# Kernel optimization log

Measured on AMD Instinct MI355X. Metric: run time of the kernel, lower is better.

The kernel has to match this reference:

```python
import jax, jax.numpy as jnp
import numpy as np

EPS = 1e-5

def _ln(x, g, b):
    mu = x.mean(-1, keepdims=True)
    v = x.var(-1, keepdims=True)
    return g * (x - mu) / jnp.sqrt(v + EPS) + b

def _mlp(x, W0, b0, g0, be0, W1, b1, g1, be1, W2, b2, nm):
    # Linear -> LN -> GELU, Linear -> LN -> GELU, Linear -> split into complex
    h = jax.nn.gelu(_ln(x @ W0 + b0, g0, be0), approximate=False)
    h = jax.nn.gelu(_ln(h @ W1 + b1, g1, be1), approximate=False)
    o = h @ W2 + b2
    return jax.lax.complex(o[..., :nm], o[..., nm:])

def _forward(x, w_W0, w_b0, w_g0, w_be0, w_W1, w_b1, w_g1, w_be1, w_W2, w_b2,
             h_W0, h_b0, h_g0, h_be0, h_W1, h_b1, h_g1, h_be1, h_W2, h_b2,
             freq_r, freq_i, mixer_w, mixer_b, norm_g, norm_b, sc_w, sc_b):
    B, C, H, W = x.shape
    m1, m2 = freq_r.shape[2], freq_r.shape[3]
    wc = jnp.linspace(0.0, 1.0, W, dtype=x.dtype)
    hc = jnp.linspace(0.0, 1.0, H, dtype=x.dtype)
    # W-basis conditioned on values and normalized w-coordinate
    x_nhwc = x.transpose(0, 2, 3, 1)                                   # (B,H,W,C)
    w_in = jnp.concatenate([x_nhwc, jnp.broadcast_to(wc[None, None, :, None], (B, H, W, 1))], -1)
    wb = _mlp(w_in, w_W0, w_b0, w_g0, w_be0, w_W1, w_b1, w_g1, w_be1, w_W2, w_b2, m2)  # (B,H,W,m2) c64
    xc = x.astype(jnp.complex64)
    t = jnp.einsum('bchw,bhwm->bchm', xc, wb)                          # (B,C,H,m2)
    # H-basis conditioned on real part of W-transformed signal
    h_in = jnp.concatenate([t.real.transpose(0, 3, 2, 1),
                            jnp.broadcast_to(hc[None, None, :, None], (B, m2, H, 1))], -1)
    hb = _mlp(h_in, h_W0, h_b0, h_g0, h_be0, h_W1, h_b1, h_g1, h_be1, h_W2, h_b2, m1)  # (B,m2,H,m1)
    t2 = jnp.einsum('bchm,bmhn->bcnm', t, hb)                          # (B,C,m1,m2)
    Wf = jax.lax.complex(freq_r, freq_i)                               # (C,O,m1,m2)
    proc = jnp.einsum('bixy,oixy->boxy', t2, Wf)                       # (B,O,m1,m2)
    # Inverse transforms via conjugate-transposed bases
    rec_h = jnp.einsum('bonm,bmhn->bohm', proc, jnp.conj(hb))          # (B,O,H,m2)
    rec = jnp.einsum('bohm,bhwm->bohw', rec_h, jnp.conj(wb))           # (B,O,H,W)
    y = rec.real / (H * W)
    y = jnp.einsum('bchw,oc->bohw', y, mixer_w) + mixer_b[None, :, None, None]
    mu = y.mean(1, keepdims=True)
    v = y.var(1, keepdims=True)
    y = norm_g[None, :, None, None] * (y - mu) / jnp.sqrt(v + EPS) + norm_b[None, :, None, None]
    y = jax.nn.gelu(y, approximate=False)
    sc = jnp.einsum('bchw,oc->bohw', x, sc_w) + sc_b[None, :, None, None]
    return jax.nn.gelu(y + sc, approximate=False)

def setup_inputs() -> dict:
    key = jax.random.key(0)
    B, C, O, H, W, M1, M2, HD = 8, 64, 64, 192, 192, 48, 48, 64
    ks = jax.random.split(key, 12)
    r = lambda k, sh, s=0.05: jax.random.normal(k, sh, jnp.float32) * s
    d = dict(x=jax.random.normal(ks[0], (B, C, H, W), jnp.float32))
    d.update(w_W0=r(ks[1], (C + 1, HD)), w_b0=jnp.zeros(HD), w_g0=jnp.ones(HD), w_be0=jnp.zeros(HD),
             w_W1=r(ks[2], (HD, HD)), w_b1=jnp.zeros(HD), w_g1=jnp.ones(HD), w_be1=jnp.zeros(HD),
             w_W2=r(ks[3], (HD, 2 * M2)), w_b2=jnp.zeros(2 * M2))
    d.update(h_W0=r(ks[4], (C + 1, HD)), h_b0=jnp.zeros(HD), h_g0=jnp.ones(HD), h_be0=jnp.zeros(HD),
             h_W1=r(ks[5], (HD, HD)), h_b1=jnp.zeros(HD), h_g1=jnp.ones(HD), h_be1=jnp.zeros(HD),
             h_W2=r(ks[6], (HD, 2 * M1)), h_b2=jnp.zeros(2 * M1))
    d.update(freq_r=r(ks[7], (C, O, M1, M2), 0.1), freq_i=r(ks[8], (C, O, M1, M2), 0.1),
             mixer_w=r(ks[9], (O, O)), mixer_b=jnp.zeros(O),
             norm_g=jnp.ones(O), norm_b=jnp.zeros(O),
             sc_w=r(ks[10], (O, C)), sc_b=jnp.zeros(O))
    return d

def reference(x, w_W0, w_b0, w_g0, w_be0, w_W1, w_b1, w_g1, w_be1, w_W2, w_b2,
              h_W0, h_b0, h_g0, h_be0, h_W1, h_b1, h_g1, h_be1, h_W2, h_b2,
              freq_r, freq_i, mixer_w, mixer_b, norm_g, norm_b, sc_w, sc_b):
    return _forward(x, w_W0, w_b0, w_g0, w_be0, w_W1, w_b1, w_g1, w_be1, w_W2, w_b2,
                    h_W0, h_b0, h_g0, h_be0, h_W1, h_b1, h_g1, h_be1, h_W2, h_b2,
                    freq_r, freq_i, mixer_w, mixer_b, norm_g, norm_b, sc_w, sc_b)
```

## Files before the change

kernel.cpp:

```cpp
#include <hip/hip_runtime.h>
#include <math.h>

#define LN_EPS 1e-5f

typedef short bf16x8 __attribute__((ext_vector_type(8)));
typedef float f32x4  __attribute__((ext_vector_type(4)));

__device__ __forceinline__ float gelu_f(float v) {
    return 0.5f * v * (1.0f + erff(v * 0.70710678118654752f));
}
__device__ __forceinline__ unsigned short f2bf(float f) {
    unsigned u = __float_as_uint(f);
    return (unsigned short)((u + 0x7fffu + ((u >> 16) & 1u)) >> 16);
}
__device__ __forceinline__ float bf2f(unsigned short h) {
    return __uint_as_float(((unsigned)h) << 16);
}

__global__ __launch_bounds__(256) void k0_swizzle(
    const float* __restrict__ wW0, const float* __restrict__ wW1, const float* __restrict__ wW2,
    const float* __restrict__ hW0, const float* __restrict__ hW1, const float* __restrict__ hW2,
    uint4* __restrict__ dst)
{
    int mat = blockIdx.x;
    const float* W; int N, ntiles, base;
    switch (mat) {
      case 0: W=wW0; N=64; ntiles=8;  base=0;    break;
      case 1: W=wW1; N=64; ntiles=8;  base=1024; break;
      case 2: W=wW2; N=96; ntiles=12; base=2048; break;
      case 3: W=hW0; N=64; ntiles=8;  base=3584; break;
      case 4: W=hW1; N=64; ntiles=8;  base=4608; break;
      default:W=hW2; N=96; ntiles=12; base=5632; break;
    }
    int lane = threadIdx.x & 63;
    for (int t = threadIdx.x >> 6; t < ntiles; t += 4) {
        int nt = t >> 1, ks = t & 1;
        int n  = nt*16 + (lane & 15);
        int k0 = ks*32 + (lane >> 4)*8;
        unsigned hi[8], lo[8];
        #pragma unroll
        for (int j = 0; j < 8; ++j) {
            float v = W[(k0 + j)*N + n];
            unsigned short h = f2bf(v);
            hi[j] = h;
            lo[j] = f2bf(v - bf2f(h));
        }
        uint4 ph, pl;
        ph.x = hi[0] | (hi[1]<<16); ph.y = hi[2] | (hi[3]<<16);
        ph.z = hi[4] | (hi[5]<<16); ph.w = hi[6] | (hi[7]<<16);
        pl.x = lo[0] | (lo[1]<<16); pl.y = lo[2] | (lo[3]<<16);
        pl.z = lo[4] | (lo[5]<<16); pl.w = lo[6] | (lo[7]<<16);
        dst[base + t*128 + lane]      = ph;
        dst[base + t*128 + 64 + lane] = pl;
    }
}

__global__ __launch_bounds__(256) void k0b_swizzle(
    const float* __restrict__ mw, const float* __restrict__ sw,
    uint4* __restrict__ dst)
{
    int mat = blockIdx.x;
    const float* W = mat ? sw : mw;
    int base = mat ? 1024 : 0;
    int lane = threadIdx.x & 63;
    for (int t = threadIdx.x >> 6; t < 8; t += 4) {
        int nt = t >> 1, ks = t & 1;
        int n  = nt*16 + (lane & 15);
        int k0 = ks*32 + (lane >> 4)*8;
        unsigned hi[8], lo[8];
        #pragma unroll
        for (int j = 0; j < 8; ++j) {
            float v = W[n*64 + (k0 + j)];
            unsigned short h = f2bf(v);
            hi[j] = h;
            lo[j] = f2bf(v - bf2f(h));
        }
        uint4 ph, pl;
        ph.x = hi[0] | (hi[1]<<16); ph.y = hi[2] | (hi[3]<<16);
        ph.z = hi[4] | (hi[5]<<16); ph.w = hi[6] | (hi[7]<<16);
        pl.x = lo[0] | (lo[1]<<16); pl.y = lo[2] | (lo[3]<<16);
        pl.z = lo[4] | (lo[5]<<16); pl.w = lo[6] | (lo[7]<<16);
        dst[base + t*128 + lane]      = ph;
        dst[base + t*128 + 64 + lane] = pl;
    }
}

template<int NT, int STRIDE>
__device__ __forceinline__ void gemm64s(
    const unsigned short* aHi, const unsigned short* aLo,
    const uint4* __restrict__ wsw, int tbase, int row, int quad, int lane,
    f32x4* acc)
{
    union U { uint4 u; bf16x8 b; };
    bf16x8 aH[2], aL[2];
    #pragma unroll
    for (int ks = 0; ks < 2; ++ks) {
        aH[ks] = *(const bf16x8*)&aHi[row*STRIDE + ks*32 + quad*8];
        aL[ks] = *(const bf16x8*)&aLo[row*STRIDE + ks*32 + quad*8];
    }
    #pragma unroll
    for (int nt = 0; nt < NT; ++nt) {
        f32x4 a = {0.f, 0.f, 0.f, 0.f};
        #pragma unroll
        for (int ks = 0; ks < 2; ++ks) {
            int t = tbase + nt*2 + ks;
            U bh, bl;
            bh.u = wsw[t*128 + lane];
            bl.u = wsw[t*128 + 64 + lane];
            a = __builtin_amdgcn_mfma_f32_16x16x32_bf16(aH[ks], bh.b, a, 0, 0, 0);
            a = __builtin_amdgcn_mfma_f32_16x16x32_bf16(aH[ks], bl.b, a, 0, 0, 0);
            a = __builtin_amdgcn_mfma_f32_16x16x32_bf16(aL[ks], bh.b, a, 0, 0, 0);
        }
        acc[nt] = a;
    }
}

template<int NT>
__device__ __forceinline__ void gemm64(
    const unsigned short* aHi, const unsigned short* aLo,
    const uint4* __restrict__ wsw, int tbase, int row, int quad, int lane,
    f32x4* acc)
{
    gemm64s<NT, 72>(aHi, aLo, wsw, tbase, row, quad, lane, acc);
}

__device__ __forceinline__ void ln_gelu_pass(
    f32x4* acc, const float* __restrict__ bias, const float* __restrict__ wrow,
    float coordBase, float coordScale,
    const float* __restrict__ gg, const float* __restrict__ bb,
    unsigned short* aHi, unsigned short* aLo, int rbase, int quad, int li)
{
    float vals[4][4];
    float s1[4] = {0,0,0,0}, s2[4] = {0,0,0,0};
    #pragma unroll
    for (int nt = 0; nt < 4; ++nt) {
        int col = nt*16 + li;
        float bv = bias[col];
        float br = wrow[col];
        #pragma unroll
        for (int rg = 0; rg < 4; ++rg) {
            float coord = (coordBase + (float)(rbase + quad*4 + rg)) * coordScale;
            float v = acc[nt][rg] + fmaf(coord, br, bv);
            vals[nt][rg] = v;
            s1[rg] += v;
            s2[rg] = fmaf(v, v, s2[rg]);
        }
    }
    #pragma unroll
    for (int d = 1; d < 16; d <<= 1) {
        #pragma unroll
        for (int rg = 0; rg < 4; ++rg) {
            s1[rg] += __shfl_xor(s1[rg], d, 64);
            s2[rg] += __shfl_xor(s2[rg], d, 64);
        }
    }
    #pragma unroll
    for (int nt = 0; nt < 4; ++nt) {
        int col = nt*16 + li;
        float gv = gg[col], bev = bb[col];
        #pragma unroll
        for (int rg = 0; rg < 4; ++rg) {
            float mu   = s1[rg] * 0.015625f;
            float rstd = rsqrtf(s2[rg]*0.015625f - mu*mu + LN_EPS);
            float v = gelu_f(fmaf((vals[nt][rg] - mu)*rstd, gv, bev));
            int r = rbase + quad*4 + rg;
            unsigned short hv = f2bf(v);
            aHi[r*72 + col] = hv;
            aLo[r*72 + col] = f2bf(v - bf2f(hv));
        }
    }
}

__device__ __forceinline__ void mlp_body(
    unsigned short* aHi, unsigned short* aLo,
    const uint4* __restrict__ wsw,
    const float* __restrict__ w0row,
    const float* __restrict__ b0, const float* __restrict__ g0, const float* __restrict__ be0,
    const float* __restrict__ b1, const float* __restrict__ g1, const float* __restrict__ be1,
    const float* __restrict__ b2,
    float coordBase,
    float* __restrict__ outR, float* __restrict__ outI, int pixBase)
{
    int tid = threadIdx.x;
    int wv = __builtin_amdgcn_readfirstlane(tid >> 6);
    int lane = tid & 63, li = lane & 15, quad = lane >> 4;
    int rbase = wv*16;
    int row = rbase + li;
    f32x4 acc[6];

    gemm64<4>(aHi, aLo, wsw, 0, row, quad, lane, acc);
    ln_gelu_pass(acc, b0, w0row, coordBase, 1.0f/191.0f, g0, be0, aHi, aLo, rbase, quad, li);
    gemm64<4>(aHi, aLo, wsw, 8, row, quad, lane, acc);
    ln_gelu_pass(acc, b1, b1, 0.f, 0.f, g1, be1, aHi, aLo, rbase, quad, li);
    gemm64<6>(aHi, aLo, wsw, 16, row, quad, lane, acc);
    #pragma unroll
    for (int nt = 0; nt < 6; ++nt) {
        int j = nt*16 + li;
        float bv = b2[j];
        #pragma unroll
        for (int rg = 0; rg < 4; ++rg) {
            float v = acc[nt][rg] + bv;
            int pix = pixBase + rbase + quad*4 + rg;
            if (nt < 3) outR[pix*48 + j]        = v;
            else        outI[pix*48 + (j - 48)] = v;
        }
    }
}

__global__ __launch_bounds__(256) void k1_mlp_w(
    const float* __restrict__ x, const float* __restrict__ W0full,
    const float* __restrict__ b0, const float* __restrict__ g0, const float* __restrict__ be0,
    const float* __restrict__ b1, const float* __restrict__ g1, const float* __restrict__ be1,
    const float* __restrict__ b2,
    const uint4* __restrict__ wsw,
    float* __restrict__ wb_r, float* __restrict__ wb_i)
{
    __shared__ unsigned short aHi[64*72];
    __shared__ unsigned short aLo[64*72];
    int tid = threadIdx.x;
    int wv = __builtin_amdgcn_readfirstlane(tid >> 6);
    int lane = tid & 63, li = lane & 15, quad = lane >> 4;
    int wq = blockIdx.x % 3;
    int bh = blockIdx.x / 3;
    int b = bh / 192, h = bh % 192;
    int w0 = wq * 64;
    int r = wv*16 + li;
    #pragma unroll
    for (int cc = 0; cc < 16; ++cc) {
        int c = cc*4 + quad;
        float v = x[((b*64 + c)*192 + h)*192 + (w0 + r)];
        unsigned short hv = f2bf(v);
        aHi[r*72 + c] = hv;
        aLo[r*72 + c] = f2bf(v - bf2f(hv));
    }
    mlp_body(aHi, aLo, wsw, W0full + 64*64, b0, g0, be0, b1, g1, be1, b2,
             (float)w0, wb_r, wb_i, bh*192 + w0);
}

__global__ __launch_bounds__(256) void k3_mlp_h(
    const float* __restrict__ t_r, const float* __restrict__ W0full,
    const float* __restrict__ b0, const float* __restrict__ g0, const float* __restrict__ be0,
    const float* __restrict__ b1, const float* __restrict__ g1, const float* __restrict__ be1,
    const float* __restrict__ b2,
    const uint4* __restrict__ wsw,
    float* __restrict__ hb_r, float* __restrict__ hb_i)
{
    __shared__ unsigned short aHi[64*72];
    __shared__ unsigned short aLo[64*72];
    int tid = threadIdx.x;
    int wv = __builtin_amdgcn_readfirstlane(tid >> 6);
    int lane = tid & 63, li = lane & 15, quad = lane >> 4;
    int hq = blockIdx.x % 3;
    int bm = blockIdx.x / 3;
    int b = bm / 48, m = bm % 48;
    int h0 = hq * 64;
    int r = wv*16 + li;
    #pragma unroll
    for (int cc = 0; cc < 16; ++cc) {
        int c = cc*4 + quad;
        float v = t_r[((b*192 + h0 + r)*64 + c)*48 + m];
        unsigned short hv = f2bf(v);
        aHi[r*72 + c] = hv;
        aLo[r*72 + c] = f2bf(v - bf2f(hv));
    }
    mlp_body(aHi, aLo, wsw, W0full + 64*64, b0, g0, be0, b1, g1, be1, b2,
             (float)h0, hb_r, hb_i, bm*192 + h0);
}

__global__ __launch_bounds__(256) void k2_t(
    const float* __restrict__ x,
    const float* __restrict__ wb_r, const float* __restrict__ wb_i,
    float* __restrict__ t_r, float* __restrict__ t_i)
{
    __shared__ unsigned short aHi[64*72];
    __shared__ unsigned short aLo[64*72];
    __shared__ uint4 bfrag[1536];
    int bh = blockIdx.x;
    int b = bh / 192, h = bh % 192;
    int tid = threadIdx.x;
    int wv = __builtin_amdgcn_readfirstlane(tid >> 6);
    int lane = tid & 63, li = lane & 15, quad = lane >> 4;
    int rbase = wv*16;
    int row = rbase + li;

    f32x4 acc[6];
    {
        f32x4 z = {0.f, 0.f, 0.f, 0.f};
        #pragma unroll
        for (int nt = 0; nt < 6; ++nt) acc[nt] = z;
    }
    union U { uint4 u; bf16x8 b8; };

    for (int w0 = 0; w0 < 192; w0 += 64) {
        if (w0) __syncthreads();
        {
            const float4* srow = (const float4*)(x + ((b*64 + row)*192 + h)*192 + w0) + quad*4;
            #pragma unroll
            for (int q = 0; q < 4; ++q) {
                float4 v4 = srow[q];
                float vv[4] = {v4.x, v4.y, v4.z, v4.w};
                int k0 = quad*16 + q*4;
                #pragma unroll
                for (int e = 0; e < 4; ++e) {
                    unsigned short hv = f2bf(vv[e]);
                    aHi[row*72 + k0 + e] = hv;
                    aLo[row*72 + k0 + e] = f2bf(vv[e] - bf2f(hv));
                }
            }
        }
        for (int t = tid >> 6; t < 12; t += 4) {
            int nt = t >> 1, ks = t & 1;
            const float* src = (nt < 3) ? wb_r : wb_i;
            int col = (nt < 3 ? nt : nt - 3)*16 + li;
            const float* sp = src + (bh*192 + w0 + ks*32 + quad*8)*48 + col;
            unsigned hi8[8], lo8[8];
            #pragma unroll
            for (int j = 0; j < 8; ++j) {
                float v = sp[j*48];
                unsigned short hv = f2bf(v);
                hi8[j] = hv;
                lo8[j] = f2bf(v - bf2f(hv));
            }
            uint4 ph, pl;
            ph.x = hi8[0] | (hi8[1]<<16); ph.y = hi8[2] | (hi8[3]<<16);
            ph.z = hi8[4] | (hi8[5]<<16); ph.w = hi8[6] | (hi8[7]<<16);
            pl.x = lo8[0] | (lo8[1]<<16); pl.y = lo8[2] | (lo8[3]<<16);
            pl.z = lo8[4] | (lo8[5]<<16); pl.w = lo8[6] | (lo8[7]<<16);
            bfrag[t*64 + lane]       = ph;
            bfrag[768 + t*64 + lane] = pl;
        }
        __syncthreads();
        bf16x8 aH[2], aL[2];
        #pragma unroll
        for (int ks = 0; ks < 2; ++ks) {
            aH[ks] = *(const bf16x8*)&aHi[row*72 + ks*32 + quad*8];
            aL[ks] = *(const bf16x8*)&aLo[row*72 + ks*32 + quad*8];
        }
        #pragma unroll
        for (int nt = 0; nt < 6; ++nt) {
            f32x4 a = acc[nt];
            #pragma unroll
            for (int ks = 0; ks < 2; ++ks) {
                int t = nt*2 + ks;
                U bh_, bl_;
                bh_.u = bfrag[t*64 + lane];
                bl_.u = bfrag[768 + t*64 + lane];
                a = __builtin_amdgcn_mfma_f32_16x16x32_bf16(aH[ks], bh_.b8, a, 0, 0, 0);
                a = __builtin_amdgcn_mfma_f32_16x16x32_bf16(aH[ks], bl_.b8, a, 0, 0, 0);
                a = __builtin_amdgcn_mfma_f32_16x16x32_bf16(aL[ks], bh_.b8, a, 0, 0, 0);
            }
            acc[nt] = a;
        }
    }
    #pragma unroll
    for (int nt = 0; nt < 6; ++nt) {
        #pragma unroll
        for (int rg = 0; rg < 4; ++rg) {
            int c = rbase + quad*4 + rg;
            float v = acc[nt][rg];
            if (nt < 3) t_r[(bh*64 + c)*48 + nt*16 + li]       = v;
            else        t_i[(bh*64 + c)*48 + (nt - 3)*16 + li] = v;
        }
    }
}

__global__ __launch_bounds__(256) void k4_t2(
    const float* __restrict__ t_r, const float* __restrict__ t_i,
    const float* __restrict__ hb_r, const float* __restrict__ hb_i,
    float* __restrict__ t2_r, float* __restrict__ t2_i)
{
    __shared__ unsigned short aHi[64*72];
    __shared__ unsigned short aLo[64*72];
    __shared__ uint4 bfrag[1536];
    int bm = blockIdx.x;
    int b = bm / 48, m = bm % 48;
    int tid = threadIdx.x;
    int wv = __builtin_amdgcn_readfirstlane(tid >> 6);
    int lane = tid & 63, li = lane & 15, quad = lane >> 4;
    int rbase = wv*16;
    int row = rbase + li;

    f32x4 acc[6];
    {
        f32x4 z = {0.f, 0.f, 0.f, 0.f};
        #pragma unroll
        for (int nt = 0; nt < 6; ++nt) acc[nt] = z;
    }
    union U { uint4 u; bf16x8 b8; };

    for (int p = 0; p < 6; ++p) {
        bool realp = (p < 3);
        int h0 = (p % 3) * 64;
        if (p) __syncthreads();
        {
            const float* tsrc = (realp ? t_r : t_i)
                              + ((b*192 + h0)*64 + row)*48 + m;
            #pragma unroll
            for (int q = 0; q < 16; ++q) {
                int k = quad*16 + q;
                float v = tsrc[k*3072];
                unsigned short hv = f2bf(v);
                aHi[row*72 + k] = hv;
                aLo[row*72 + k] = f2bf(v - bf2f(hv));
            }
        }
        for (int t = tid >> 6; t < 12; t += 4) {
            int nt = t >> 1, ks = t & 1;
            const float* src;
            int col;
            float sgn = 1.f;
            if (realp) {
                if (nt < 3) { src = hb_r; col = nt*16 + li; }
                else        { src = hb_i; col = (nt - 3)*16 + li; }
            } else {
                if (nt < 3) { src = hb_i; col = nt*16 + li; sgn = -1.f; }
                else        { src = hb_r; col = (nt - 3)*16 + li; }
            }
            const float* sp = src + (bm*192 + h0 + ks*32 + quad*8)*48 + col;
            unsigned hi8[8], lo8[8];
            #pragma unroll
            for (int j = 0; j < 8; ++j) {
                float v = sgn * sp[j*48];
                unsigned short hv = f2bf(v);
                hi8[j] = hv;
                lo8[j] = f2bf(v - bf2f(hv));
            }
            uint4 ph, pl;
            ph.x = hi8[0] | (hi8[1]<<16); ph.y = hi8[2] | (hi8[3]<<16);
            ph.z = hi8[4] | (hi8[5]<<16); ph.w = hi8[6] | (hi8[7]<<16);
            pl.x = lo8[0] | (lo8[1]<<16); pl.y = lo8[2] | (lo8[3]<<16);
            pl.z = lo8[4] | (lo8[5]<<16); pl.w = lo8[6] | (lo8[7]<<16);
            bfrag[t*64 + lane]       = ph;
            bfrag[768 + t*64 + lane] = pl;
        }
        __syncthreads();
        bf16x8 aH[2], aL[2];
        #pragma unroll
        for (int ks = 0; ks < 2; ++ks) {
            aH[ks] = *(const bf16x8*)&aHi[row*72 + ks*32 + quad*8];
            aL[ks] = *(const bf16x8*)&aLo[row*72 + ks*32 + quad*8];
        }
        #pragma unroll
        for (int nt = 0; nt < 6; ++nt) {
            f32x4 a = acc[nt];
            #pragma unroll
            for (int ks = 0; ks < 2; ++ks) {
                int t = nt*2 + ks;
                U bh_, bl_;
                bh_.u = bfrag[t*64 + lane];
                bl_.u = bfrag[768 + t*64 + lane];
                a = __builtin_amdgcn_mfma_f32_16x16x32_bf16(aH[ks], bh_.b8, a, 0, 0, 0);
                a = __builtin_amdgcn_mfma_f32_16x16x32_bf16(aH[ks], bl_.b8, a, 0, 0, 0);
                a = __builtin_amdgcn_mfma_f32_16x16x32_bf16(aL[ks], bh_.b8, a, 0, 0, 0);
            }
            acc[nt] = a;
        }
    }
    #pragma unroll
    for (int nt = 0; nt < 6; ++nt) {
        #pragma unroll
        for (int rg = 0; rg < 4; ++rg) {
            int c = rbase + quad*4 + rg;
            float v = acc[nt][rg];
            if (nt < 3) t2_r[((b*64 + c)*48 + nt*16 + li)*48 + m]       = v;
            else        t2_i[((b*64 + c)*48 + (nt - 3)*16 + li)*48 + m] = v;
        }
    }
}

__global__ __launch_bounds__(256) void k5_proc(
    const float* __restrict__ t2_r, const float* __restrict__ t2_i,
    const float* __restrict__ fr, const float* __restrict__ fi,
    float* __restrict__ proc_r, float* __restrict__ proc_i)
{
    int og = blockIdx.x & 31;
    int ch = blockIdx.x >> 5;
    int nm = ch*256 + threadIdx.x;
    int o0 = og*2;
    float p0r[8], p0i[8], p1r[8], p1i[8];
    #pragma unroll
    for (int bb = 0; bb < 8; ++bb) { p0r[bb]=0.f; p0i[bb]=0.f; p1r[bb]=0.f; p1i[bb]=0.f; }
    for (int i = 0; i < 64; ++i) {
        float w0r = fr[(o0*64 + i)*2304 + nm];
        float w0i = fi[(o0*64 + i)*2304 + nm];
        float w1r = fr[((o0+1)*64 + i)*2304 + nm];
        float w1i = fi[((o0+1)*64 + i)*2304 + nm];
        #pragma unroll
        for (int bb = 0; bb < 8; ++bb) {
            float tr = t2_r[(bb*64 + i)*2304 + nm];
            float ti = t2_i[(bb*64 + i)*2304 + nm];
            p0r[bb] = fmaf(tr, w0r, fmaf(-ti, w0i, p0r[bb]));
            p0i[bb] = fmaf(tr, w0i, fmaf( ti, w0r, p0i[bb]));
            p1r[bb] = fmaf(tr, w1r, fmaf(-ti, w1i, p1r[bb]));
            p1i[bb] = fmaf(tr, w1i, fmaf( ti, w1r, p1i[bb]));
        }
    }
    #pragma unroll
    for (int bb = 0; bb < 8; ++bb) {
        proc_r[(bb*64 + o0)*2304 + nm]     = p0r[bb];
        proc_i[(bb*64 + o0)*2304 + nm]     = p0i[bb];
        proc_r[(bb*64 + o0 + 1)*2304 + nm] = p1r[bb];
        proc_i[(bb*64 + o0 + 1)*2304 + nm] = p1i[bb];
    }
}

__global__ __launch_bounds__(256) void k6_rech(
    const float* __restrict__ proc_r, const float* __restrict__ proc_i,
    const float* __restrict__ hb_r, const float* __restrict__ hb_i,
    float* __restrict__ rh_r, float* __restrict__ rh_i)
{
    __shared__ unsigned short aHi[64*104];
    __shared__ unsigned short aLo[64*104];
    __shared__ uint4 bfrag[1536];
    int hq = blockIdx.x % 3;
    int bm = blockIdx.x / 3;
    int b = bm / 48, m = bm % 48;
    int h0 = hq * 64;
    int tid = threadIdx.x;
    int wv = __builtin_amdgcn_readfirstlane(tid >> 6);
    int lane = tid & 63, li = lane & 15, quad = lane >> 4;
    int rbase = wv*16;
    int row = rbase + li;

    {
        int hr = bm*192 + h0 + row;
        const float4* pr = (const float4*)(hb_r + hr*48) + quad*3;
        const float4* pi = (const float4*)(hb_i + hr*48) + quad*3;
        #pragma unroll
        for (int q = 0; q < 3; ++q) {
            float4 vr = pr[q];
            float4 vi = pi[q];
            int k0 = quad*12 + q*4;
            float vs[8] = {vr.x, vr.y, vr.z, vr.w, vi.x, vi.y, vi.z, vi.w};
            #pragma unroll
            for (int e = 0; e < 4; ++e) {
                unsigned short h1 = f2bf(vs[e]);
                aHi[row*104 + k0 + e] = h1;
                aLo[row*104 + k0 + e] = f2bf(vs[e] - bf2f(h1));
                unsigned short h2 = f2bf(vs[4+e]);
                aHi[row*104 + 48 + k0 + e] = h2;
                aLo[row*104 + 48 + k0 + e] = f2bf(vs[4+e] - bf2f(h2));
            }
        }
    }
    union U { uint4 u; bf16x8 b8; };
    bf16x8 aH[3], aL[3];
    #pragma unroll
    for (int ks = 0; ks < 3; ++ks) {
        aH[ks] = *(const bf16x8*)&aHi[row*104 + ks*32 + quad*8];
        aL[ks] = *(const bf16x8*)&aLo[row*104 + ks*32 + quad*8];
    }

    f32x4 accR[4], accI[4];
    for (int pass = 0; pass < 2; ++pass) {
        if (pass) __syncthreads();
        for (int t = tid >> 6; t < 12; t += 4) {
            int ks = t % 3;
            int nt = t / 3;
            int o = nt*16 + li;
            const float* base_lo = pass ? proc_i : proc_r;
            const float* base_hi = pass ? proc_r : proc_i;
            float sgn_hi = pass ? -1.f : 1.f;
            unsigned hi8[8], lo8[8];
            #pragma unroll
            for (int j = 0; j < 8; ++j) {
                int kk = ks*32 + quad*8 + j;
                float v;
                if (kk < 48) v = base_lo[(b*64 + o)*2304 + kk*48 + m];
                else         v = sgn_hi * base_hi[(b*64 + o)*2304 + (kk - 48)*48 + m];
                unsigned short hv = f2bf(v);
                hi8[j] = hv;
                lo8[j] = f2bf(v - bf2f(hv));
            }
            uint4 ph, pl;
            ph.x = hi8[0] | (hi8[1]<<16); ph.y = hi8[2] | (hi8[3]<<16);
            ph.z = hi8[4] | (hi8[5]<<16); ph.w = hi8[6] | (hi8[7]<<16);
            pl.x = lo8[0] | (lo8[1]<<16); pl.y = lo8[2] | (lo8[3]<<16);
            pl.z = lo8[4] | (lo8[5]<<16); pl.w = lo8[6] | (lo8[7]<<16);
            bfrag[t*64 + lane]       = ph;
            bfrag[768 + t*64 + lane] = pl;
        }
        __syncthreads();
        f32x4* acc = pass ? accI : accR;
        #pragma unroll
        for (int nt = 0; nt < 4; ++nt) {
            f32x4 a = {0.f, 0.f, 0.f, 0.f};
            #pragma unroll
            for (int ks = 0; ks < 3; ++ks) {
                int t = nt*3 + ks;
                U bh_, bl_;
                bh_.u = bfrag[t*64 + lane];
                bl_.u = bfrag[768 + t*64 + lane];
                a = __builtin_amdgcn_mfma_f32_16x16x32_bf16(aH[ks], bh_.b8, a, 0, 0, 0);
                a = __builtin_amdgcn_mfma_f32_16x16x32_bf16(aH[ks], bl_.b8, a, 0, 0, 0);
                a = __builtin_amdgcn_mfma_f32_16x16x32_bf16(aL[ks], bh_.b8, a, 0, 0, 0);
            }
            acc[nt] = a;
        }
    }
    #pragma unroll
    for (int nt = 0; nt < 4; ++nt) {
        int o = nt*16 + li;
        #pragma unroll
        for (int rg = 0; rg < 4; ++rg) {
            int hrow = h0 + rbase + quad*4 + rg;
            int a = (bm*192 + hrow)*64 + o;
            rh_r[a] = accR[nt][rg];
            rh_i[a] = accI[nt][rg];
        }
    }
}

__global__ __launch_bounds__(256) void k7_rec(
    const float* __restrict__ rh_r, const float* __restrict__ rh_i,
    const float* __restrict__ wb_r, const float* __restrict__ wb_i,
    const float* __restrict__ x,
    const uint4* __restrict__ msw,
    const float* __restrict__ mb,
    const float* __restrict__ nrm_g, const float* __restrict__ nrm_b,
    const float* __restrict__ sb,
    float* __restrict__ out)
{
    __shared__ unsigned short aHi[64*104];
    __shared__ unsigned short aLo[64*104];
    __shared__ uint4 bfrag[1536];
    float* cbuf = (float*)bfrag;

    int wq = blockIdx.x % 3;
    int bh = blockIdx.x / 3;
    int b = bh / 192, h = bh % 192;
    int w0 = wq * 64;
    int tid = threadIdx.x;
    int wv = __builtin_amdgcn_readfirstlane(tid >> 6);
    int lane = tid & 63, li = lane & 15, quad = lane >> 4;
    int rbase = wv*16;
    int row = rbase + li;

    {
        int pix = bh*192 + w0 + row;
        const float4* pr = (const float4*)(wb_r + pix*48) + quad*3;
        const float4* pi = (const float4*)(wb_i + pix*48) + quad*3;
        #pragma unroll
        for (int q = 0; q < 3; ++q) {
            float4 vr = pr[q];
            float4 vi = pi[q];
            int k0 = quad*12 + q*4;
            float vs[8] = {vr.x, vr.y, vr.z, vr.w, vi.x, vi.y, vi.z, vi.w};
            #pragma unroll
            for (int e = 0; e < 4; ++e) {
                unsigned short h1 = f2bf(vs[e]);
                aHi[row*104 + k0 + e] = h1;
                aLo[row*104 + k0 + e] = f2bf(vs[e] - bf2f(h1));
                unsigned short h2 = f2bf(vs[4+e]);
                aHi[row*104 + 48 + k0 + e] = h2;
                aLo[row*104 + 48 + k0 + e] = f2bf(vs[4+e] - bf2f(h2));
            }
        }
    }
    for (int t = tid >> 6; t < 12; t += 4) {
        int ks = t % 3;
        int nt = t / 3;
        int o = nt*16 + li;
        unsigned hi8[8], lo8[8];
        #pragma unroll
        for (int j = 0; j < 8; ++j) {
            int kk = ks*32 + quad*8 + j;
            const float* src = (kk < 48) ? rh_r : rh_i;
            int m = (kk < 48) ? kk : kk - 48;
            float v = src[((b*48 + m)*192 + h)*64 + o];
            unsigned short hv = f2bf(v);
            hi8[j] = hv;
            lo8[j] = f2bf(v - bf2f(hv));
        }
        uint4 ph, pl;
        ph.x = hi8[0] | (hi8[1]<<16); ph.y = hi8[2] | (hi8[3]<<16);
        ph.z = hi8[4] | (hi8[5]<<16); ph.w = hi8[6] | (hi8[7]<<16);
        pl.x = lo8[0] | (lo8[1]<<16); pl.y = lo8[2] | (lo8[3]<<16);
        pl.z = lo8[4] | (lo8[5]<<16); pl.w = lo8[6] | (lo8[7]<<16);
        bfrag[t*64 + lane]       = ph;
        bfrag[768 + t*64 + lane] = pl;
    }
    __syncthreads();

    union U { uint4 u; bf16x8 b; };
    bf16x8 aH[3], aL[3];
    #pragma unroll
    for (int ks = 0; ks < 3; ++ks) {
        aH[ks] = *(const bf16x8*)&aHi[row*104 + ks*32 + quad*8];
        aL[ks] = *(const bf16x8*)&aLo[row*104 + ks*32 + quad*8];
    }
    f32x4 acc[4];
    #pragma unroll
    for (int nt = 0; nt < 4; ++nt) {
        f32x4 a = {0.f, 0.f, 0.f, 0.f};
        #pragma unroll
        for (int ks = 0; ks < 3; ++ks) {
            int t = nt*3 + ks;
            U bh_, bl_;
            bh_.u = bfrag[t*64 + lane];
            bl_.u = bfrag[768 + t*64 + lane];
            a = __builtin_amdgcn_mfma_f32_16x16x32_bf16(aH[ks], bh_.b, a, 0, 0, 0);
            a = __builtin_amdgcn_mfma_f32_16x16x32_bf16(aH[ks], bl_.b, a, 0, 0, 0);
            a = __builtin_amdgcn_mfma_f32_16x16x32_bf16(aL[ks], bh_.b, a, 0, 0, 0);
        }
        acc[nt] = a;
    }

    const float s = 1.0f / 36864.0f;
    #pragma unroll
    for (int nt = 0; nt < 4; ++nt) {
        int o = nt*16 + li;
        #pragma unroll
        for (int rg = 0; rg < 4; ++rg) {
            int prow = rbase + quad*4 + rg;
            float v = acc[nt][rg] * s;
            unsigned short hv = f2bf(v);
            aHi[prow*104 + o] = hv;
            aLo[prow*104 + o] = f2bf(v - bf2f(hv));
        }
    }
    f32x4 accy[4];
    gemm64s<4, 104>(aHi, aLo, msw, 0, row, quad, lane, accy);

    float vals[4][4];
    float s1[4] = {0,0,0,0}, s2[4] = {0,0,0,0};
    #pragma unroll
    for (int nt = 0; nt < 4; ++nt) {
        int o = nt*16 + li;
        float bv = mb[o];
        #pragma unroll
        for (int rg = 0; rg < 4; ++rg) {
            float v = accy[nt][rg] + bv;
            vals[nt][rg] = v;
            s1[rg] += v;
            s2[rg] = fmaf(v, v, s2[rg]);
        }
    }
    #pragma unroll
    for (int d = 1; d < 16; d <<= 1) {
        #pragma unroll
        for (int rg = 0; rg < 4; ++rg) {
            s1[rg] += __shfl_xor(s1[rg], d, 64);
            s2[rg] += __shfl_xor(s2[rg], d, 64);
        }
    }

    #pragma unroll
    for (int cc = 0; cc < 16; ++cc) {
        int c = cc*4 + quad;
        float v = x[((b*64 + c)*192 + h)*192 + w0 + row];
        unsigned short hv = f2bf(v);
        aHi[row*104 + c] = hv;
        aLo[row*104 + c] = f2bf(v - bf2f(hv));
    }
    gemm64s<4, 104>(aHi, aLo, msw, 8, row, quad, lane, acc);

    __syncthreads();
    #pragma unroll
    for (int nt = 0; nt < 4; ++nt) {
        int o = nt*16 + li;
        float gv = nrm_g[o], bev = nrm_b[o], sbv = sb[o];
        #pragma unroll
        for (int rg = 0; rg < 4; ++rg) {
            float mu   = s1[rg] * 0.015625f;
            float rstd = rsqrtf(s2[rg]*0.015625f - mu*mu + LN_EPS);
            float v  = gelu_f(fmaf((vals[nt][rg] - mu)*rstd, gv, bev));
            float sc = acc[nt][rg] + sbv;
            int prow = rbase + quad*4 + rg;
            cbuf[prow*67 + o] = gelu_f(v + sc);
        }
    }
    __syncthreads();
    #pragma unroll
    for (int it = 0; it < 16; ++it) {
        int o = it*4 + (tid >> 6);
        int pix = tid & 63;
        out[((b*64 + o)*192 + h)*192 + w0 + pix] = cbuf[pix*67 + o];
    }
}

extern "C" void kernel_launch(void* const* d_in, const int* in_sizes, int n_in,
                              void* d_out, int out_size, void* d_ws, size_t ws_size,
                              hipStream_t stream)
{
    (void)in_sizes; (void)n_in; (void)out_size; (void)ws_size;
    const float* x    = (const float*)d_in[0];
    const float* wW0  = (const float*)d_in[1];
    const float* wb0  = (const float*)d_in[2];
    const float* wg0  = (const float*)d_in[3];
    const float* wbe0 = (const float*)d_in[4];
    const float* wW1  = (const float*)d_in[5];
    const float* wb1  = (const float*)d_in[6];
    const float* wg1  = (const float*)d_in[7];
    const float* wbe1 = (const float*)d_in[8];
    const float* wW2  = (const float*)d_in[9];
    const float* wb2  = (const float*)d_in[10];
    const float* hW0  = (const float*)d_in[11];
    const float* hb0  = (const float*)d_in[12];
    const float* hg0  = (const float*)d_in[13];
    const float* hbe0 = (const float*)d_in[14];
    const float* hW1  = (const float*)d_in[15];
    const float* hb1  = (const float*)d_in[16];
    const float* hg1  = (const float*)d_in[17];
    const float* hbe1 = (const float*)d_in[18];
    const float* hW2  = (const float*)d_in[19];
    const float* hb2  = (const float*)d_in[20];
    const float* fr   = (const float*)d_in[21];
    const float* fi   = (const float*)d_in[22];
    const float* mw   = (const float*)d_in[23];
    const float* mb   = (const float*)d_in[24];
    const float* ngp  = (const float*)d_in[25];
    const float* nbp  = (const float*)d_in[26];
    const float* sw   = (const float*)d_in[27];
    const float* sb   = (const float*)d_in[28];
    float* out = (float*)d_out;

    float* ws   = (float*)d_ws;
    float* wbr  = ws;
    float* wbi  = ws + 14155776;
    float* t_r  = ws + 28311552;
    float* t_i  = ws + 33030144;
    float* hbr  = ws + 37748736;
    float* hbi  = ws + 41287680;
    float* t2r  = ws + 44826624;
    float* t2i  = ws + 46006272;
    float* prr  = ws + 47185920;
    float* pri  = ws + 48365568;
    float* rhr  = t_r;
    float* rhi  = t_i;
    float* wswb = ws + 49545216;
    uint4* wsw  = (uint4*)wswb;
    uint4* msw  = (uint4*)t2r;

    k0_swizzle<<<dim3(6), dim3(256), 0, stream>>>(wW0, wW1, wW2, hW0, hW1, hW2, wsw);
    k1_mlp_w<<<dim3(4608), dim3(256), 0, stream>>>(x, wW0, wb0, wg0, wbe0,
                                                   wb1, wg1, wbe1, wb2, wsw, wbr, wbi);
    k2_t<<<dim3(1536), dim3(256), 0, stream>>>(x, wbr, wbi, t_r, t_i);
    k3_mlp_h<<<dim3(1152), dim3(256), 0, stream>>>(t_r, hW0, hb0, hg0, hbe0,
                                                   hb1, hg1, hbe1, hb2, wsw + 3584, hbr, hbi);
    k4_t2<<<dim3(384), dim3(256), 0, stream>>>(t_r, t_i, hbr, hbi, t2r, t2i);
    k5_proc<<<dim3(288), dim3(256), 0, stream>>>(t2r, t2i, fr, fi, prr, pri);
    k0b_swizzle<<<dim3(2), dim3(256), 0, stream>>>(mw, sw, msw);
    k6_rech<<<dim3(1152), dim3(256), 0, stream>>>(prr, pri, hbr, hbi, rhr, rhi);
    k7_rec<<<dim3(4608), dim3(256), 0, stream>>>(rhr, rhi, wbr, wbi,
                                                 x, msw, mb, ngp, nbp, sb, out);
}
```

Measured before the change: 685.0 us.

## Transpose t and proc intermediate layouts for coalesced loads downstream

Changes the storage layout of the intermediate t (now b,m,h,c) and proc (now b,m,o,n) so that the consumers k3, k4 and k6 read contiguous data, using float4 loads in k3 and k6. k2 now stages its output through shared memory, reusing the bfrag buffer, so its writes into the new layout stay coalesced. k5 writes proc with a strided pattern in exchange. The aim is to remove the heavily strided gathers in the MLP-H, t2 and rec_h kernels, at the cost of extra barriers in k2 and less coalesced stores in k5.

New measurement: 567.8 us. 17.1% less time.

```diff
diff --git a/kernel.cpp b/kernel.cpp
--- a/kernel.cpp
+++ b/kernel.cpp
@@ -255,13 +255,20 @@
     int b = bm / 48, m = bm % 48;
     int h0 = hq * 64;
     int r = wv*16 + li;
-    #pragma unroll
-    for (int cc = 0; cc < 16; ++cc) {
-        int c = cc*4 + quad;
-        float v = t_r[((b*192 + h0 + r)*64 + c)*48 + m];
-        unsigned short hv = f2bf(v);
-        aHi[r*72 + c] = hv;
-        aLo[r*72 + c] = f2bf(v - bf2f(hv));
+    {
+        const float4* tb = (const float4*)(t_r + ((b*48 + m)*192 + h0 + r)*64);
+        #pragma unroll
+        for (int q = 0; q < 4; ++q) {
+            float4 v4 = tb[quad*4 + q];
+            float vv[4] = {v4.x, v4.y, v4.z, v4.w};
+            int k0 = quad*16 + q*4;
+            #pragma unroll
+            for (int e = 0; e < 4; ++e) {
+                unsigned short hv = f2bf(vv[e]);
+                aHi[r*72 + k0 + e] = hv;
+                aLo[r*72 + k0 + e] = f2bf(vv[e] - bf2f(hv));
+            }
+        }
     }
     mlp_body(aHi, aLo, wsw, W0full + 64*64, b0, g0, be0, b1, g1, be1, b2,
              (float)h0, hb_r, hb_i, bm*192 + h0);
@@ -275,6 +282,7 @@
     __shared__ unsigned short aHi[64*72];
     __shared__ unsigned short aLo[64*72];
     __shared__ uint4 bfrag[1536];
+    float* cbuf = (float*)bfrag;
     int bh = blockIdx.x;
     int b = bh / 192, h = bh % 192;
     int tid = threadIdx.x;
@@ -352,15 +360,35 @@
             acc[nt] = a;
         }
     }
-    #pragma unroll
-    for (int nt = 0; nt < 6; ++nt) {
+    __syncthreads();
+    #pragma unroll
+    for (int nt = 0; nt < 3; ++nt) {
+        int m = nt*16 + li;
         #pragma unroll
         for (int rg = 0; rg < 4; ++rg) {
             int c = rbase + quad*4 + rg;
-            float v = acc[nt][rg];
-            if (nt < 3) t_r[(bh*64 + c)*48 + nt*16 + li]       = v;
-            else        t_i[(bh*64 + c)*48 + (nt - 3)*16 + li] = v;
-        }
+            cbuf[m*67 + c] = acc[nt][rg];
+        }
+    }
+    __syncthreads();
+    for (int idx = tid; idx < 3072; idx += 256) {
+        int m = idx >> 6, c = idx & 63;
+        t_r[((b*48 + m)*192 + h)*64 + c] = cbuf[m*67 + c];
+    }
+    __syncthreads();
+    #pragma unroll
+    for (int nt = 3; nt < 6; ++nt) {
+        int m = (nt - 3)*16 + li;
+        #pragma unroll
+        for (int rg = 0; rg < 4; ++rg) {
+            int c = rbase + quad*4 + rg;
+            cbuf[m*67 + c] = acc[nt][rg];
+        }
+    }
+    __syncthreads();
+    for (int idx = tid; idx < 3072; idx += 256) {
+        int m = idx >> 6, c = idx & 63;
+        t_i[((b*48 + m)*192 + h)*64 + c] = cbuf[m*67 + c];
     }
 }
 
@@ -393,12 +421,11 @@
         int h0 = (p % 3) * 64;
         if (p) __syncthreads();
         {
-            const float* tsrc = (realp ? t_r : t_i)
-                              + ((b*192 + h0)*64 + row)*48 + m;
+            const float* tsrc = (realp ? t_r : t_i) + ((b*48 + m)*192 + h0)*64 + row;
             #pragma unroll
             for (int q = 0; q < 16; ++q) {
                 int k = quad*16 + q;
-                float v = tsrc[k*3072];
+                float v = tsrc[k*64];
                 unsigned short hv = f2bf(v);
                 aHi[row*72 + k] = hv;
                 aLo[row*72 + k] = f2bf(v - bf2f(hv));
@@ -476,6 +503,7 @@
     int og = blockIdx.x & 31;
     int ch = blockIdx.x >> 5;
     int nm = ch*256 + threadIdx.x;
+    int n = nm / 48, mm = nm % 48;
     int o0 = og*2;
     float p0r[8], p0i[8], p1r[8], p1i[8];
     #pragma unroll
@@ -497,10 +525,11 @@
     }
     #pragma unroll
     for (int bb = 0; bb < 8; ++bb) {
-        proc_r[(bb*64 + o0)*2304 + nm]     = p0r[bb];
-        proc_i[(bb*64 + o0)*2304 + nm]     = p0i[bb];
-        proc_r[(bb*64 + o0 + 1)*2304 + nm] = p1r[bb];
-        proc_i[(bb*64 + o0 + 1)*2304 + nm] = p1i[bb];
+        int base0 = ((bb*48 + mm)*64 + o0)*48 + n;
+        proc_r[base0]      = p0r[bb];
+        proc_i[base0]      = p0i[bb];
+        proc_r[base0 + 48] = p1r[bb];
+        proc_i[base0 + 48] = p1i[bb];
     }
 }
 
@@ -558,16 +587,20 @@
             int ks = t % 3;
             int nt = t / 3;
             int o = nt*16 + li;
-            const float* base_lo = pass ? proc_i : proc_r;
-            const float* base_hi = pass ? proc_r : proc_i;
-            float sgn_hi = pass ? -1.f : 1.f;
+            int kk0 = ks*32 + quad*8;
+            const float* srcp;
+            int n0;
+            float sgn;
+            if (kk0 < 48) { srcp = pass ? proc_i : proc_r; n0 = kk0;      sgn = 1.f; }
+            else          { srcp = pass ? proc_r : proc_i; n0 = kk0 - 48; sgn = pass ? -1.f : 1.f; }
+            const float* sp = srcp + ((b*48 + m)*64 + o)*48 + n0;
+            float4 f0 = *(const float4*)sp;
+            float4 f1 = *(const float4*)(sp + 4);
+            float vv[8] = {f0.x, f0.y, f0.z, f0.w, f1.x, f1.y, f1.z, f1.w};
             unsigned hi8[8], lo8[8];
             #pragma unroll
             for (int j = 0; j < 8; ++j) {
-                int kk = ks*32 + quad*8 + j;
-                float v;
-                if (kk < 48) v = base_lo[(b*64 + o)*2304 + kk*48 + m];
-                else         v = sgn_hi * base_hi[(b*64 + o)*2304 + (kk - 48)*48 + m];
+                float v = sgn * vv[j];
                 unsigned short hv = f2bf(v);
                 hi8[j] = hv;
                 lo8[j] = f2bf(v - bf2f(hv));
```
